# Performance work log

Measured on AMD Instinct MI355X. Metric: run time of the kernel, lower is better.

Reference implementation:

```python
import jax, jax.numpy as jnp
import numpy as np

N = 50000      # nodes
E = 800000     # edges (avg degree 16)
IN = 512       # input features
OUT = 32       # per-head hidden features
H = 8          # heads (layer 1)
C = 16         # classes (layer 2, 1 head)
NEG_SLOPE = 0.2


def setup_inputs() -> dict:
    key = jax.random.key(0)
    ks = jax.random.split(key, 8)
    x = jax.random.normal(ks[0], (N, IN), jnp.float32)
    edge_index = jax.random.randint(ks[1], (2, E), 0, N, jnp.int32)
    # layer 1 params: W1 [IN, H*OUT], attention vectors a1_src/a1_dst [H, OUT]
    W1 = jax.random.normal(ks[2], (IN, H * OUT), jnp.float32) * (1.0 / np.sqrt(IN))
    a1_src = jax.random.normal(ks[3], (H, OUT), jnp.float32) * (1.0 / np.sqrt(OUT))
    a1_dst = jax.random.normal(ks[4], (H, OUT), jnp.float32) * (1.0 / np.sqrt(OUT))
    # layer 2 params: single head, W2 [H*OUT, C], a2_src/a2_dst [1, C]
    W2 = jax.random.normal(ks[5], (H * OUT, C), jnp.float32) * (1.0 / np.sqrt(H * OUT))
    a2_src = jax.random.normal(ks[6], (1, C), jnp.float32) * (1.0 / np.sqrt(C))
    a2_dst = jax.random.normal(ks[7], (1, C), jnp.float32) * (1.0 / np.sqrt(C))
    return {"x": x, "W1": W1, "a1_src": a1_src, "a1_dst": a1_dst,
            "W2": W2, "a2_src": a2_src, "a2_dst": a2_dst,
            "edge_index": edge_index}


def gat_layer(x, edge_index, W, a_src, a_dst, concat):
    """Standard GAT layer: e_ij = LeakyReLU(a_src.Wh_i + a_dst.Wh_j),
    softmax over incoming edges of each target node, scatter-aggregate."""
    n = x.shape[0]
    h_heads, f = a_src.shape
    h = (x @ W).reshape(n, h_heads, f)                      # [N, H, F]
    src, dst = edge_index[0], edge_index[1]
    es = jnp.einsum('nhf,hf->nh', h, a_src)                 # [N, H] per-node src scores
    ed = jnp.einsum('nhf,hf->nh', h, a_dst)                 # [N, H]
    e = jax.nn.leaky_relu(es[src] + ed[dst], NEG_SLOPE)     # [E, H] per-edge logits
    # segment softmax over edges grouped by dst node
    m = jax.ops.segment_max(e, dst, num_segments=n)         # [N, H]
    m = jnp.where(jnp.isfinite(m), m, 0.0)                  # empty segments -> -inf
    p = jnp.exp(e - m[dst])                                 # [E, H]
    s = jax.ops.segment_sum(p, dst, num_segments=n)         # [N, H]
    denom = s[dst]
    alpha = p / jnp.where(denom > 0, denom, 1.0)            # [E, H]
    msg = h[src] * alpha[:, :, None]                        # [E, H, F]
    out = jax.ops.segment_sum(msg, dst, num_segments=n)     # [N, H, F]
    if concat:
        return out.reshape(n, h_heads * f)
    return out.mean(axis=1)


def reference(x, W1, a1_src, a1_dst, W2, a2_src, a2_dst, edge_index):
    # dropout is identity in eval mode
    h = gat_layer(x, edge_index, W1, a1_src, a1_dst, concat=True)   # [N, H*OUT]
    h = jax.nn.elu(h)
    h = gat_layer(h, edge_index, W2, a2_src, a2_dst, concat=False)  # [N, C]
    return jax.nn.log_softmax(h, axis=1)
```

## Files before the change

kernel.cpp:

```cpp
#include <hip/hip_runtime.h>

#define NN 50000
#define EE 800000
#define KIN 512
#define HF 256
#define NH 8
#define FOUT 32
#define NC 16
#define NEG 0.2f
#define NB_SCAN 196

typedef unsigned short u16;
typedef __attribute__((ext_vector_type(8))) short shortx8;
typedef __attribute__((ext_vector_type(4))) float floatx4;
typedef __attribute__((ext_vector_type(8))) unsigned short ushortx8;
typedef __attribute__((ext_vector_type(4))) unsigned uintx4;

__device__ __forceinline__ float lrelu(float x) { return x > 0.f ? x : NEG * x; }

__device__ __forceinline__ u16 f2bf(float f) {
    unsigned u = __float_as_uint(f);
    return (u16)((u + 0x7FFFu + ((u >> 16) & 1u)) >> 16);
}
__device__ __forceinline__ float bf2f(u16 v) {
    return __uint_as_float((unsigned)v << 16);
}
__device__ __forceinline__ unsigned pk2bf(float a, float b) {
    unsigned ua = __float_as_uint(a), ub = __float_as_uint(b);
    return ((ua + 0x8000u) >> 16) | ((ub + 0x8000u) & 0xffff0000u);
}

__device__ __forceinline__ void gll16(const void* g, void* l) {
    __builtin_amdgcn_global_load_lds((const __attribute__((address_space(1))) void*)g,
                                     (__attribute__((address_space(3))) void*)l, 16, 0, 0);
}

__global__ void count_deg(const int* __restrict__ dst, int* __restrict__ deg) {
    int e = blockIdx.x * 256 + threadIdx.x;
    if (e < EE) atomicAdd(&deg[dst[e]], 1);
}

__global__ __launch_bounds__(256) void scan_a(const int* __restrict__ deg, int* __restrict__ bsum) {
    __shared__ int sm[256];
    int t = threadIdx.x;
    int i = blockIdx.x * 256 + t;
    sm[t] = (i < NN) ? deg[i] : 0;
    __syncthreads();
    for (int o = 128; o; o >>= 1) { if (t < o) sm[t] += sm[t + o]; __syncthreads(); }
    if (t == 0) bsum[blockIdx.x] = sm[0];
}

__global__ __launch_bounds__(256) void scan_b(const int* __restrict__ bsum, int* __restrict__ boff) {
    __shared__ int sm[256];
    int t = threadIdx.x;
    sm[t] = (t < NB_SCAN) ? bsum[t] : 0;
    __syncthreads();
    for (int d = 1; d < 256; d <<= 1) {
        int v = (t >= d) ? sm[t - d] : 0;
        __syncthreads();
        sm[t] += v;
        __syncthreads();
    }
    if (t < NB_SCAN) boff[t] = (t == 0) ? 0 : sm[t - 1];
}

__global__ __launch_bounds__(256) void scan_c(const int* __restrict__ deg, const int* __restrict__ boff,
                                              int* __restrict__ off) {
    __shared__ int sm[256];
    int t = threadIdx.x;
    int i = blockIdx.x * 256 + t;
    int d = (i < NN) ? deg[i] : 0;
    sm[t] = d;
    __syncthreads();
    for (int dd = 1; dd < 256; dd <<= 1) {
        int v = (t >= dd) ? sm[t - dd] : 0;
        __syncthreads();
        sm[t] += v;
        __syncthreads();
    }
    if (i < NN) off[i] = boff[blockIdx.x] + sm[t] - d;
    if (i == 0) off[NN] = EE;
}

__global__ void fill_csr(const int* __restrict__ src, const int* __restrict__ dst,
                         const int* __restrict__ off, int* __restrict__ cursor,
                         int* __restrict__ csr_src) {
    int e = blockIdx.x * 256 + threadIdx.x;
    if (e < EE) {
        int d = dst[e];
        int pos = atomicAdd(&cursor[d], 1);
        csr_src[off[d] + pos] = src[e];
    }
}

__global__ __launch_bounds__(256) void convert_w(const float* __restrict__ W1, const float* __restrict__ W2,
                                                 u16* __restrict__ w1t, u16* __restrict__ w2t) {
    int e = blockIdx.x * 256 + threadIdx.x;
    if (e < KIN * HF) {
        int k = e >> 8, n = e & 255;
        w1t[n * KIN + k] = f2bf(W1[e]);
    } else {
        int e2 = e - KIN * HF;
        if (e2 < HF * NC) {
            int k = e2 >> 4, c = e2 & 15;
            w2t[c * HF + k] = f2bf(W2[e2]);
        }
    }
}

__global__ __launch_bounds__(256, 2) void gemm1_mfma(const float* __restrict__ x,
                                                     const u16* __restrict__ w1t,
                                                     u16* __restrict__ h1b) {
    __shared__ __align__(16) float As[128 * 32];
    __shared__ __align__(16) u16 Bs[256 * 32];
    int t = threadIdx.x;
    int lane = t & 63, wave = t >> 6;
    int wm = wave >> 1, wn = wave & 1;
    int lm = lane & 15, quad = lane >> 4;
    int bm = blockIdx.x * 128;

    floatx4 acc[4][8];
#pragma unroll
    for (int i = 0; i < 4; i++)
#pragma unroll
        for (int j = 0; j < 8; j++) acc[i][j] = (floatx4){0.f, 0.f, 0.f, 0.f};

    int arow_l = wave * 32 + (lane >> 3);
    int akoff = (lane & 7) * 4;
    const float* aptr[4];
#pragma unroll
    for (int i = 0; i < 4; i++) {
        int ar = bm + arow_l + i * 8;
        if (ar > NN - 1) ar = NN - 1;
        aptr[i] = x + (size_t)ar * KIN + akoff;
    }
    float* alds[4];
#pragma unroll
    for (int i = 0; i < 4; i++) alds[i] = As + (wave * 32 + i * 8) * 32;

    int brow_l = wave * 64 + (lane >> 2);
    int bkoff = (lane & 3) * 8;
    const u16* bptr[4];
#pragma unroll
    for (int i = 0; i < 4; i++) bptr[i] = w1t + (size_t)(brow_l + i * 16) * KIN + bkoff;
    u16* blds[4];
#pragma unroll
    for (int i = 0; i < 4; i++) blds[i] = Bs + (wave * 64 + i * 16) * 32;

    int offA[4], offB[8];
#pragma unroll
    for (int i = 0; i < 4; i++) offA[i] = (wm * 64 + i * 16 + lm) * 32 + quad * 8;
#pragma unroll
    for (int j = 0; j < 8; j++) offB[j] = (wn * 128 + j * 16 + lm) * 32 + quad * 8;

    for (int kk = 0; kk < KIN; kk += 32) {
#pragma unroll
        for (int i = 0; i < 4; i++) gll16(aptr[i] + kk, alds[i]);
#pragma unroll
        for (int i = 0; i < 4; i++) gll16(bptr[i] + kk, blds[i]);
        __syncthreads();
        shortx8 af[4], bf[8];
#pragma unroll
        for (int i = 0; i < 4; i++) {
            const float4* ap = (const float4*)&As[offA[i]];
            float4 lo = ap[0], hi = ap[1];
            union { uintx4 u; shortx8 s; } cv;
            cv.u[0] = pk2bf(lo.x, lo.y);
            cv.u[1] = pk2bf(lo.z, lo.w);
            cv.u[2] = pk2bf(hi.x, hi.y);
            cv.u[3] = pk2bf(hi.z, hi.w);
            af[i] = cv.s;
        }
#pragma unroll
        for (int j = 0; j < 8; j++) bf[j] = *(const shortx8*)&Bs[offB[j]];
#pragma unroll
        for (int i = 0; i < 4; i++)
#pragma unroll
            for (int j = 0; j < 8; j++)
                acc[i][j] = __builtin_amdgcn_mfma_f32_16x16x32_bf16(af[i], bf[j], acc[i][j], 0, 0, 0);
        __syncthreads();
    }

#pragma unroll
    for (int i = 0; i < 4; i++) {
        int row = bm + wm * 64 + i * 16 + quad * 4;
#pragma unroll
        for (int j = 0; j < 8; j++) {
            int col = wn * 128 + j * 16 + lm;
#pragma unroll
            for (int r = 0; r < 4; r++) {
                if (row + r < NN) h1b[(size_t)(row + r) * HF + col] = f2bf(acc[i][j][r]);
            }
        }
    }
}

__global__ __launch_bounds__(256) void scores1(const u16* __restrict__ h1b, const float* __restrict__ a_src,
                                               const float* __restrict__ a_dst,
                                               float* __restrict__ es, float* __restrict__ ed) {
    __shared__ float as_s[HF], ad_s[HF];
    int t = threadIdx.x;
    as_s[t] = a_src[t];
    ad_s[t] = a_dst[t];
    __syncthreads();
    int nl = t >> 5;
    int L = t & 31;
    int n = blockIdx.x * 8 + nl;
    ushortx8 hv = *(const ushortx8*)(h1b + (size_t)n * HF + L * 8);
    float ps = 0.f, pd = 0.f;
#pragma unroll
    for (int i = 0; i < 8; i++) {
        float v = bf2f(hv[i]);
        ps += v * as_s[L * 8 + i];
        pd += v * ad_s[L * 8 + i];
    }
    ps += __shfl_down(ps, 2, 4); ps += __shfl_down(ps, 1, 4);
    pd += __shfl_down(pd, 2, 4); pd += __shfl_down(pd, 1, 4);
    if ((L & 3) == 0) {
        int h = L >> 2;
        es[n * NH + h] = ps;
        ed[n * NH + h] = pd;
    }
}

__global__ __launch_bounds__(256) void agg1(const u16* __restrict__ h1b, const float* __restrict__ es,
                                            const float* __restrict__ ed, const int* __restrict__ off,
                                            const int* __restrict__ csr_src, u16* __restrict__ out1b) {
    int wave = threadIdx.x >> 6;
    int lane = threadIdx.x & 63;
    int n = blockIdx.x * 4 + wave;
    int fh = lane & 31;
    int ep = lane >> 5;
    int head = fh >> 2;
    int beg = off[n];
    int deg = off[n + 1] - beg;
    float edh = ed[n * NH + head];
    const u16* hbase = h1b + fh * 8;
    float acc[8] = {0.f, 0.f, 0.f, 0.f, 0.f, 0.f, 0.f, 0.f};
    float s_part = 0.f;
    for (int base = 0; base < deg; base += 16) {
        int nch = deg - base; if (nch > 16) nch = 16;
        int sv = (lane < nch) ? csr_src[beg + base + lane] : 0;
#pragma unroll
        for (int e = 0; e < 8; e++) {
            int ee = 2 * e + ep;
            int s = __shfl(sv, ee, 64);
            if (ee < nch) {
                float lg = es[s * NH + head] + edh;
                float p = __expf(lg > 0.f ? lg : NEG * lg);
                ushortx8 hv = *(const ushortx8*)(hbase + (size_t)s * HF);
                s_part += p;
#pragma unroll
                for (int i = 0; i < 8; i++) acc[i] += p * bf2f(hv[i]);
            }
        }
    }
#pragma unroll
    for (int i = 0; i < 8; i++) acc[i] += __shfl_down(acc[i], 32, 64);
    s_part += __shfl_down(s_part, 32, 64);
    if (lane < 32) {
        float inv = s_part > 0.f ? 1.0f / s_part : 0.f;
        union { uintx4 u; ushortx8 v; } ob;
#pragma unroll
        for (int i = 0; i < 4; i++) {
            float v0 = acc[2 * i] * inv, v1 = acc[2 * i + 1] * inv;
            v0 = v0 > 0.f ? v0 : (__expf(v0) - 1.0f);
            v1 = v1 > 0.f ? v1 : (__expf(v1) - 1.0f);
            ob.u[i] = (unsigned)f2bf(v0) | ((unsigned)f2bf(v1) << 16);
        }
        *(ushortx8*)(out1b + (size_t)n * HF + fh * 8) = ob.v;
    }
}

__global__ __launch_bounds__(64) void gemm2_mfma(const u16* __restrict__ out1b, const u16* __restrict__ w2t,
                                                 const float* __restrict__ a2s, const float* __restrict__ a2d,
                                                 float* __restrict__ h2, float* __restrict__ es2,
                                                 float* __restrict__ ed2) {
    int lane = threadIdx.x;
    int lm = lane & 15, quad = lane >> 4;
    int nb = blockIdx.x * 16;
    floatx4 acc = (floatx4){0.f, 0.f, 0.f, 0.f};
    const u16* arow = out1b + (size_t)(nb + lm) * HF + quad * 8;
    const u16* brow = w2t + lm * HF + quad * 8;
#pragma unroll
    for (int kk = 0; kk < HF; kk += 32) {
        shortx8 af = *(const shortx8*)(arow + kk);
        shortx8 bf = *(const shortx8*)(brow + kk);
        acc = __builtin_amdgcn_mfma_f32_16x16x32_bf16(af, bf, acc, 0, 0, 0);
    }
    float a2sc = a2s[lm], a2dc = a2d[lm];
#pragma unroll
    for (int r = 0; r < 4; r++) {
        int n = nb + quad * 4 + r;
        float v = acc[r];
        h2[n * NC + lm] = v;
        float ps = v * a2sc, pd = v * a2dc;
#pragma unroll
        for (int o = 8; o; o >>= 1) {
            ps += __shfl_down(ps, o, 16);
            pd += __shfl_down(pd, o, 16);
        }
        if (lm == 0) { es2[n] = ps; ed2[n] = pd; }
    }
}

__global__ __launch_bounds__(256) void agg2(const float* __restrict__ h2, const float* __restrict__ es2,
                                            const float* __restrict__ ed2, const int* __restrict__ off,
                                            const int* __restrict__ csr_src, float* __restrict__ out) {
    int t = threadIdx.x;
    int nid = blockIdx.x * 16 + (t >> 4);
    int c = t & 15;
    int beg = off[nid];
    int deg = off[nid + 1] - beg;
    float edn = ed2[nid];
    float s = 0.f, acc = 0.f;
    for (int base = 0; base < deg; base += 16) {
        int nch = deg - base; if (nch > 16) nch = 16;
        int sv = 0;
        if (c < nch) sv = csr_src[beg + base + c];
        int sva[16];
#pragma unroll
        for (int e = 0; e < 16; e++) sva[e] = __shfl(sv, e, 16);
        float hva[16];
#pragma unroll
        for (int e = 0; e < 16; e++) hva[e] = h2[sva[e] * NC + c];
        float p = 0.f;
        if (c < nch) p = __expf(lrelu(es2[sv] + edn));
        s += p;
        float pa[16];
#pragma unroll
        for (int e = 0; e < 16; e++) pa[e] = __shfl(p, e, 16);
#pragma unroll
        for (int e = 0; e < 16; e++) acc += pa[e] * hva[e];
    }
#pragma unroll
    for (int o = 8; o; o >>= 1) s += __shfl_down(s, o, 16);
    s = __shfl(s, 0, 16);
    float v = (s > 0.f) ? acc / s : 0.f;
    float m2 = v;
#pragma unroll
    for (int o = 8; o; o >>= 1) m2 = fmaxf(m2, __shfl_down(m2, o, 16));
    m2 = __shfl(m2, 0, 16);
    float se = __expf(v - m2);
#pragma unroll
    for (int o = 8; o; o >>= 1) se += __shfl_down(se, o, 16);
    se = __shfl(se, 0, 16);
    out[nid * NC + c] = v - m2 - __logf(se);
}

extern "C" void kernel_launch(void* const* d_in, const int* in_sizes, int n_in,
                              void* d_out, int out_size, void* d_ws, size_t ws_size,
                              hipStream_t stream) {
    const float* x   = (const float*)d_in[0];
    const float* W1  = (const float*)d_in[1];
    const float* a1s = (const float*)d_in[2];
    const float* a1d = (const float*)d_in[3];
    const float* W2  = (const float*)d_in[4];
    const float* a2s = (const float*)d_in[5];
    const float* a2d = (const float*)d_in[6];
    const int*   ei  = (const int*)d_in[7];
    const int* srcv = ei;
    const int* dstv = ei + EE;
    float* out = (float*)d_out;

    u16* h1b    = (u16*)d_ws;
    u16* out1b  = h1b + (size_t)NN * HF;
    float* es1  = (float*)(out1b + (size_t)NN * HF);
    float* ed1  = es1 + (size_t)NN * NH;
    float* h2   = ed1 + (size_t)NN * NH;
    float* es2v = h2 + (size_t)NN * NC;
    float* ed2v = es2v + NN;
    int* deg    = (int*)(ed2v + NN);
    int* cursor = deg + NN;
    int* offs   = cursor + NN;
    int* csr    = offs + NN + 1;
    int* bsum   = csr + EE;
    int* boff   = bsum + 256;
    u16* w1t    = (u16*)(boff + 256);
    u16* w2t    = w1t + (size_t)HF * KIN;

    hipMemsetAsync(deg, 0, 2 * NN * sizeof(int), stream);
    count_deg<<<(EE + 255) / 256, 256, 0, stream>>>(dstv, deg);
    scan_a<<<NB_SCAN, 256, 0, stream>>>(deg, bsum);
    scan_b<<<1, 256, 0, stream>>>(bsum, boff);
    scan_c<<<NB_SCAN, 256, 0, stream>>>(deg, boff, offs);
    fill_csr<<<(EE + 255) / 256, 256, 0, stream>>>(srcv, dstv, offs, cursor, csr);
    convert_w<<<(KIN * HF + HF * NC + 255) / 256, 256, 0, stream>>>(W1, W2, w1t, w2t);
    gemm1_mfma<<<(NN + 127) / 128, 256, 0, stream>>>(x, w1t, h1b);
    scores1<<<NN / 8, 256, 0, stream>>>(h1b, a1s, a1d, es1, ed1);
    agg1<<<NN / 4, 256, 0, stream>>>(h1b, es1, ed1, offs, csr, out1b);
    gemm2_mfma<<<NN / 16, 64, 0, stream>>>(out1b, w2t, a2s, a2d, h2, es2v, ed2v);
    agg2<<<NN / 16, 256, 0, stream>>>(h2, es2v, ed2v, offs, csr, out);
}
```

Before: 360.7 us.

## Fuse attention scores into GEMM1 epilogue, merge weight conversion, reshape agg1 per-head

```diff
diff --git a/kernel.cpp b/kernel.cpp
--- a/kernel.cpp
+++ b/kernel.cpp
@@ -14,6 +14,7 @@
 typedef __attribute__((ext_vector_type(8))) short shortx8;
 typedef __attribute__((ext_vector_type(4))) float floatx4;
 typedef __attribute__((ext_vector_type(8))) unsigned short ushortx8;
+typedef __attribute__((ext_vector_type(4))) unsigned short ushortx4;
 typedef __attribute__((ext_vector_type(4))) unsigned uintx4;
 
 __device__ __forceinline__ float lrelu(float x) { return x > 0.f ? x : NEG * x; }
@@ -35,9 +36,19 @@
                                      (__attribute__((address_space(3))) void*)l, 16, 0, 0);
 }
 
-__global__ void count_deg(const int* __restrict__ dst, int* __restrict__ deg) {
+__global__ void count_deg_convw(const int* __restrict__ dst, int* __restrict__ deg,
+                                const float* __restrict__ W1, const float* __restrict__ W2,
+                                u16* __restrict__ w1t, u16* __restrict__ w2t) {
     int e = blockIdx.x * 256 + threadIdx.x;
     if (e < EE) atomicAdd(&deg[dst[e]], 1);
+    if (e < KIN * HF) {
+        int k = e >> 8, n = e & 255;
+        w1t[n * KIN + k] = f2bf(W1[e]);
+    } else if (e < KIN * HF + HF * NC) {
+        int e2 = e - KIN * HF;
+        int k = e2 >> 4, c = e2 & 15;
+        w2t[c * HF + k] = f2bf(W2[e2]);
+    }
 }
 
 __global__ __launch_bounds__(256) void scan_a(const int* __restrict__ deg, int* __restrict__ bsum) {
@@ -93,24 +104,13 @@
     }
 }
 
-__global__ __launch_bounds__(256) void convert_w(const float* __restrict__ W1, const float* __restrict__ W2,
-                                                 u16* __restrict__ w1t, u16* __restrict__ w2t) {
-    int e = blockIdx.x * 256 + threadIdx.x;
-    if (e < KIN * HF) {
-        int k = e >> 8, n = e & 255;
-        w1t[n * KIN + k] = f2bf(W1[e]);
-    } else {
-        int e2 = e - KIN * HF;
-        if (e2 < HF * NC) {
-            int k = e2 >> 4, c = e2 & 15;
-            w2t[c * HF + k] = f2bf(W2[e2]);
-        }
-    }
-}
-
 __global__ __launch_bounds__(256, 2) void gemm1_mfma(const float* __restrict__ x,
                                                      const u16* __restrict__ w1t,
-                                                     u16* __restrict__ h1b) {
+                                                     u16* __restrict__ h1b,
+                                                     const float* __restrict__ a1s,
+                                                     const float* __restrict__ a1d,
+                                                     float* __restrict__ est,
+                                                     float* __restrict__ edt) {
     __shared__ __align__(16) float As[128 * 32];
     __shared__ __align__(16) u16 Bs[256 * 32];
     int t = threadIdx.x;
@@ -193,82 +193,91 @@
             }
         }
     }
-}
-
-__global__ __launch_bounds__(256) void scores1(const u16* __restrict__ h1b, const float* __restrict__ a_src,
-                                               const float* __restrict__ a_dst,
-                                               float* __restrict__ es, float* __restrict__ ed) {
-    __shared__ float as_s[HF], ad_s[HF];
-    int t = threadIdx.x;
-    as_s[t] = a_src[t];
-    ad_s[t] = a_dst[t];
-    __syncthreads();
-    int nl = t >> 5;
-    int L = t & 31;
-    int n = blockIdx.x * 8 + nl;
-    ushortx8 hv = *(const ushortx8*)(h1b + (size_t)n * HF + L * 8);
-    float ps = 0.f, pd = 0.f;
-#pragma unroll
-    for (int i = 0; i < 8; i++) {
-        float v = bf2f(hv[i]);
-        ps += v * as_s[L * 8 + i];
-        pd += v * ad_s[L * 8 + i];
-    }
-    ps += __shfl_down(ps, 2, 4); ps += __shfl_down(ps, 1, 4);
-    pd += __shfl_down(pd, 2, 4); pd += __shfl_down(pd, 1, 4);
-    if ((L & 3) == 0) {
-        int h = L >> 2;
-        es[n * NH + h] = ps;
-        ed[n * NH + h] = pd;
-    }
-}
-
-__global__ __launch_bounds__(256) void agg1(const u16* __restrict__ h1b, const float* __restrict__ es,
-                                            const float* __restrict__ ed, const int* __restrict__ off,
+
+    float as_v[8], ad_v[8];
+#pragma unroll
+    for (int j = 0; j < 8; j++) {
+        int col = wn * 128 + j * 16 + lm;
+        as_v[j] = a1s[col];
+        ad_v[j] = a1d[col];
+    }
+#pragma unroll
+    for (int i = 0; i < 4; i++) {
+#pragma unroll
+        for (int r = 0; r < 4; r++) {
+            int row = bm + wm * 64 + i * 16 + quad * 4 + r;
+#pragma unroll
+            for (int hp = 0; hp < 4; hp++) {
+                float e_s = acc[i][2 * hp][r] * as_v[2 * hp] + acc[i][2 * hp + 1][r] * as_v[2 * hp + 1];
+                float e_d = acc[i][2 * hp][r] * ad_v[2 * hp] + acc[i][2 * hp + 1][r] * ad_v[2 * hp + 1];
+#pragma unroll
+                for (int o = 8; o; o >>= 1) {
+                    e_s += __shfl_down(e_s, o, 16);
+                    e_d += __shfl_down(e_d, o, 16);
+                }
+                if (lm == 0 && row < NN) {
+                    int h = wn * 4 + hp;
+                    est[(size_t)h * NN + row] = e_s;
+                    edt[(size_t)h * NN + row] = e_d;
+                }
+            }
+        }
+    }
+}
+
+__global__ __launch_bounds__(256) void agg1(const u16* __restrict__ h1b, const float* __restrict__ est,
+                                            const float* __restrict__ edt, const int* __restrict__ off,
                                             const int* __restrict__ csr_src, u16* __restrict__ out1b) {
+    int head = blockIdx.x & 7;
+    int grp  = blockIdx.x >> 3;
     int wave = threadIdx.x >> 6;
     int lane = threadIdx.x & 63;
-    int n = blockIdx.x * 4 + wave;
-    int fh = lane & 31;
-    int ep = lane >> 5;
-    int head = fh >> 2;
-    int beg = off[n];
-    int deg = off[n + 1] - beg;
-    float edh = ed[n * NH + head];
-    const u16* hbase = h1b + fh * 8;
-    float acc[8] = {0.f, 0.f, 0.f, 0.f, 0.f, 0.f, 0.f, 0.f};
-    float s_part = 0.f;
-    for (int base = 0; base < deg; base += 16) {
-        int nch = deg - base; if (nch > 16) nch = 16;
-        int sv = (lane < nch) ? csr_src[beg + base + lane] : 0;
-#pragma unroll
-        for (int e = 0; e < 8; e++) {
-            int ee = 2 * e + ep;
-            int s = __shfl(sv, ee, 64);
-            if (ee < nch) {
-                float lg = es[s * NH + head] + edh;
+    int slot = lane >> 3;
+    int fq   = lane & 7;
+    const float* esh = est + (size_t)head * NN;
+    const float* edh_p = edt + (size_t)head * NN;
+    const u16* hbase = h1b + head * 32 + fq * 4;
+#pragma unroll
+    for (int rep = 0; rep < 2; rep++) {
+        int n = grp * 8 + wave * 2 + rep;
+        int beg = off[n];
+        int deg = off[n + 1] - beg;
+        float edh = edh_p[n];
+        float a0 = 0.f, a1 = 0.f, a2 = 0.f, a3 = 0.f, sp = 0.f;
+        for (int base = 0; base < deg; base += 8) {
+            int sv = (lane < 8 && base + lane < deg) ? csr_src[beg + base + lane] : 0;
+            int s = __shfl(sv, slot, 64);
+            if (base + slot < deg) {
+                float lg = esh[s] + edh;
                 float p = __expf(lg > 0.f ? lg : NEG * lg);
-                ushortx8 hv = *(const ushortx8*)(hbase + (size_t)s * HF);
-                s_part += p;
-#pragma unroll
-                for (int i = 0; i < 8; i++) acc[i] += p * bf2f(hv[i]);
+                ushortx4 hv = *(const ushortx4*)(hbase + (size_t)s * HF);
+                sp += p;
+                a0 += p * bf2f(hv[0]);
+                a1 += p * bf2f(hv[1]);
+                a2 += p * bf2f(hv[2]);
+                a3 += p * bf2f(hv[3]);
             }
         }
-    }
-#pragma unroll
-    for (int i = 0; i < 8; i++) acc[i] += __shfl_down(acc[i], 32, 64);
-    s_part += __shfl_down(s_part, 32, 64);
-    if (lane < 32) {
-        float inv = s_part > 0.f ? 1.0f / s_part : 0.f;
-        union { uintx4 u; ushortx8 v; } ob;
-#pragma unroll
-        for (int i = 0; i < 4; i++) {
-            float v0 = acc[2 * i] * inv, v1 = acc[2 * i + 1] * inv;
+#pragma unroll
+        for (int o = 32; o >= 8; o >>= 1) {
+            a0 += __shfl_down(a0, o, 64);
+            a1 += __shfl_down(a1, o, 64);
+            a2 += __shfl_down(a2, o, 64);
+            a3 += __shfl_down(a3, o, 64);
+            sp += __shfl_down(sp, o, 64);
+        }
+        if (lane < 8) {
+            float inv = sp > 0.f ? 1.0f / sp : 0.f;
+            float v0 = a0 * inv, v1 = a1 * inv, v2 = a2 * inv, v3 = a3 * inv;
             v0 = v0 > 0.f ? v0 : (__expf(v0) - 1.0f);
             v1 = v1 > 0.f ? v1 : (__expf(v1) - 1.0f);
-            ob.u[i] = (unsigned)f2bf(v0) | ((unsigned)f2bf(v1) << 16);
-        }
-        *(ushortx8*)(out1b + (size_t)n * HF + fh * 8) = ob.v;
+            v2 = v2 > 0.f ? v2 : (__expf(v2) - 1.0f);
+            v3 = v3 > 0.f ? v3 : (__expf(v3) - 1.0f);
+            uint2 ob;
+            ob.x = (unsigned)f2bf(v0) | ((unsigned)f2bf(v1) << 16);
+            ob.y = (unsigned)f2bf(v2) | ((unsigned)f2bf(v3) << 16);
+            *(uint2*)(out1b + (size_t)n * HF + head * 32 + fq * 4) = ob;
+        }
     }
 }
 
@@ -365,9 +374,9 @@
 
     u16* h1b    = (u16*)d_ws;
     u16* out1b  = h1b + (size_t)NN * HF;
-    float* es1  = (float*)(out1b + (size_t)NN * HF);
-    float* ed1  = es1 + (size_t)NN * NH;
-    float* h2   = ed1 + (size_t)NN * NH;
+    float* est  = (float*)(out1b + (size_t)NN * HF);
+    float* edt  = est + (size_t)NH * NN;
+    float* h2   = edt + (size_t)NH * NN;
     float* es2v = h2 + (size_t)NN * NC;
     float* ed2v = es2v + NN;
     int* deg    = (int*)(ed2v + NN);
@@ -380,15 +389,13 @@
     u16* w2t    = w1t + (size_t)HF * KIN;
 
     hipMemsetAsync(deg, 0, 2 * NN * sizeof(int), stream);
-    count_deg<<<(EE + 255) / 256, 256, 0, stream>>>(dstv, deg);
+    count_deg_convw<<<(EE + 255) / 256, 256, 0, stream>>>(dstv, deg, W1, W2, w1t, w2t);
     scan_a<<<NB_SCAN, 256, 0, stream>>>(deg, bsum);
     scan_b<<<1, 256, 0, stream>>>(bsum, boff);
     scan_c<<<NB_SCAN, 256, 0, stream>>>(deg, boff, offs);
     fill_csr<<<(EE + 255) / 256, 256, 0, stream>>>(srcv, dstv, offs, cursor, csr);
-    convert_w<<<(KIN * HF + HF * NC + 255) / 256, 256, 0, stream>>>(W1, W2, w1t, w2t);
-    gemm1_mfma<<<(NN + 127) / 128, 256, 0, stream>>>(x, w1t, h1b);
-    scores1<<<NN / 8, 256, 0, stream>>>(h1b, a1s, a1d, es1, ed1);
-    agg1<<<NN / 4, 256, 0, stream>>>(h1b, es1, ed1, offs, csr, out1b);
+    gemm1_mfma<<<(NN + 127) / 128, 256, 0, stream>>>(x, w1t, h1b, a1s, a1d, est, edt);
+    agg1<<<(NN / 8) * 8, 256, 0, stream>>>(h1b, est, edt, offs, csr, out1b);
     gemm2_mfma<<<NN / 16, 64, 0, stream>>>(out1b, w2t, a2s, a2d, h2, es2v, ed2v);
     agg2<<<NN / 16, 256, 0, stream>>>(h2, es2v, ed2v, offs, csr, out);
 }
```

After: 444.8 us. +23.3%, slower.
